# Performance work log

Hardware: AMD Instinct MI355X
Metric: run time of the kernel (lower is better)

## Reference

```python
import jax, jax.numpy as jnp
import numpy as np

B, T, V, N, H, L = 8, 512, 50257, 768, 12, 12
DH = N // H


def layernorm(x, w, eps=1e-5):
    mu = jnp.mean(x, axis=-1, keepdims=True)
    var = jnp.var(x, axis=-1, keepdims=True)
    return (x - mu) * jax.lax.rsqrt(var + eps) * w


def setup_inputs() -> dict:
    key = jax.random.key(0)
    ks = jax.random.split(key, 10)
    s = 0.02
    proj_s = 0.02 / np.sqrt(2.0)  # c_proj.weight special init (2 * n_layer, n_layer=1)
    return {
        "idx": jax.random.randint(ks[0], (B, T), 0, V),
        "wte": jax.random.normal(ks[1], (V, N), jnp.float32) * s,
        "wpe": jax.random.normal(ks[2], (T, N), jnp.float32) * s,
        "step_emb": jax.random.normal(ks[3], (L, N), jnp.float32) * s,
        "ln1_w": jnp.ones((N,), jnp.float32),
        "ln2_w": jnp.ones((N,), jnp.float32),
        "lnf_w": jnp.ones((N,), jnp.float32),
        "c_attn": jax.random.normal(ks[4], (N, 3 * N), jnp.float32) * s,
        "attn_proj": jax.random.normal(ks[5], (N, N), jnp.float32) * proj_s,
        "c_fc": jax.random.normal(ks[6], (N, 4 * N), jnp.float32) * s,
        "mlp_proj": jax.random.normal(ks[7], (4 * N, N), jnp.float32) * proj_s,
    }


def reference(idx, wte, wpe, step_emb, ln1_w, ln2_w, lnf_w, c_attn, attn_proj, c_fc, mlp_proj):
    b, t = idx.shape
    # token + position embeddings (dropout is identity in eval)
    x0 = wte[idx] + wpe[:t][None, :, :]  # [b, t, N]
    causal = jnp.tril(jnp.ones((t, t), dtype=bool))  # [t, t]
    neg_inf = jnp.finfo(x0.dtype).min

    def block(x):
        # causal self-attention
        h = layernorm(x, ln1_w)
        qkv = h @ c_attn  # [b, t, 3N]
        q, k, v = jnp.split(qkv, 3, axis=-1)
        q = q.reshape(b, t, H, DH)
        k = k.reshape(b, t, H, DH)
        v = v.reshape(b, t, H, DH)
        att = jnp.einsum('bqhd,bkhd->bhqk', q, k) / np.sqrt(DH)
        att = jnp.where(causal[None, None, :, :], att, neg_inf)
        att = jax.nn.softmax(att, axis=-1)
        y = jnp.einsum('bhqk,bkhd->bqhd', att, v).reshape(b, t, N)
        x = x + y @ attn_proj
        # MLP (exact GELU, matching torch nn.GELU default)
        m = layernorm(x, ln2_w)
        x = x + jax.nn.gelu(m @ c_fc, approximate=False) @ mlp_proj
        return x

    def step(h, se):
        h_in = h + x0 + se[None, None, :]
        return block(h_in), None

    h_final, _ = jax.lax.scan(step, x0, step_emb)  # loop num_loops times
    h_final = layernorm(h_final, lnf_w)
    # eval path with targets=None: logits only for last position, tied lm_head
    logits = h_final[:, -1:, :] @ wte.T  # [b, 1, V]
    return logits
```

## Files before the change

kernel.cpp:

```cpp
#include <hip/hip_runtime.h>
#include <hip/hip_bf16.h>
#include <math.h>

#define BB 8
#define TT 512
#define VV 50257
#define NN 768
#define HH 12
#define LL 12
#define MM (BB*TT)

typedef short bf16x8 __attribute__((ext_vector_type(8)));
typedef float f32x4 __attribute__((ext_vector_type(4)));
typedef unsigned short us8 __attribute__((ext_vector_type(8)));

__device__ __forceinline__ float bf2f(unsigned short u) {
    union { unsigned int i; float f; } x; x.i = ((unsigned int)u) << 16; return x.f;
}
__device__ __forceinline__ unsigned short f2bf(float f) {
    union { __hip_bfloat16 h; unsigned short u; } c; c.h = __float2bfloat16(f); return c.u;
}

__device__ __forceinline__ float gelu_f(float v) {
    float z = v * 0.70710678118654752f;
    float az = fabsf(z);
    float t = __builtin_amdgcn_rcpf(1.0f + 0.3275911f * az);
    float poly = t * (0.254829592f + t * (-0.284496736f + t * (1.421413741f
               + t * (-1.453152027f + t * 1.061405429f))));
    float erfa = 1.0f - poly * __expf(-z * z);
    float erfv = copysignf(erfa, z);
    return 0.5f * v * (1.0f + erfv);
}

__global__ __launch_bounds__(512) void embed_kernel(const int* __restrict__ idx,
                                                    const float* __restrict__ wte,
                                                    const float* __restrict__ wpe,
                                                    const float* __restrict__ se0,
                                                    float* __restrict__ x0,
                                                    float* __restrict__ hin)
{
    int row = blockIdx.x * 8 + (threadIdx.x >> 6);
    int lane = threadIdx.x & 63;
    int t = row % TT;
    int tok = idx[row];
    const float* wt = wte + (size_t)tok * NN;
    const float* wp = wpe + (size_t)t * NN;
    float* px = x0 + (size_t)row * NN;
    float* ph = hin + (size_t)row * NN;
#pragma unroll
    for (int i = 0; i < 3; ++i) {
        int c = (lane + i * 64) * 4;
        float4 a = *(const float4*)&wt[c];
        float4 b = *(const float4*)&wp[c];
        float4 e = *(const float4*)&se0[c];
        float4 v = make_float4(a.x + b.x, a.y + b.y, a.z + b.z, a.w + b.w);
        *(float4*)&px[c] = v;
        float4 h2 = make_float4(2.f * v.x + e.x, 2.f * v.y + e.y,
                                2.f * v.z + e.z, 2.f * v.w + e.w);
        *(float4*)&ph[c] = h2;
    }
}

__global__ __launch_bounds__(256) void wconv_all(
    const float* __restrict__ c_attn, const float* __restrict__ attn_proj,
    const float* __restrict__ c_fc, const float* __restrict__ mlp_proj,
    unsigned short* __restrict__ o1, unsigned short* __restrict__ o2,
    unsigned short* __restrict__ o3, unsigned short* __restrict__ o4)
{
    int bid = blockIdx.x;
    const float* W; unsigned short* Wt; int K, Nc, id;
    if (bid < 1728)      { W = c_attn;    Wt = o1; K = 768;  Nc = 2304; id = bid; }
    else if (bid < 2304) { W = attn_proj; Wt = o2; K = 768;  Nc = 768;  id = bid - 1728; }
    else if (bid < 4608) { W = c_fc;      Wt = o3; K = 768;  Nc = 3072; id = bid - 2304; }
    else                 { W = mlp_proj;  Wt = o4; K = 3072; Nc = 768;  id = bid - 4608; }
    int nbx = Nc / 32;
    int n0 = (id % nbx) * 32, k0 = (id / nbx) * 32;

    __shared__ float tile[32][33];
    int tid = threadIdx.x;
    int r = tid >> 3, c4 = (tid & 7) * 4;
    float4 v = *(const float4*)&W[(size_t)(k0 + r) * Nc + n0 + c4];
    tile[r][c4 + 0] = v.x; tile[r][c4 + 1] = v.y;
    tile[r][c4 + 2] = v.z; tile[r][c4 + 3] = v.w;
    __syncthreads();
    ushort4 o;
    o.x = f2bf(tile[c4 + 0][r]); o.y = f2bf(tile[c4 + 1][r]);
    o.z = f2bf(tile[c4 + 2][r]); o.w = f2bf(tile[c4 + 3][r]);
    *(ushort4*)&Wt[(size_t)(n0 + r) * K + k0 + c4] = o;
}

__global__ __launch_bounds__(512) void ln_kernel(
    const float* __restrict__ src, const float* __restrict__ w,
    unsigned short* __restrict__ out)
{
    int row = blockIdx.x * 8 + (threadIdx.x >> 6);
    int lane = threadIdx.x & 63;
    size_t base = (size_t)row * NN;
    float4 v[3];
    float s = 0.f, ss = 0.f;
#pragma unroll
    for (int i = 0; i < 3; ++i) {
        int c = (lane + i * 64) * 4;
        v[i] = *(const float4*)&src[base + c];
        s  += v[i].x + v[i].y + v[i].z + v[i].w;
        ss += v[i].x * v[i].x + v[i].y * v[i].y + v[i].z * v[i].z + v[i].w * v[i].w;
    }
#pragma unroll
    for (int off = 32; off; off >>= 1) { s += __shfl_xor(s, off); ss += __shfl_xor(ss, off); }
    float mu = s / (float)NN;
    float var = ss / (float)NN - mu * mu;
    float rsig = rsqrtf(var + 1e-5f);
#pragma unroll
    for (int i = 0; i < 3; ++i) {
        int c = (lane + i * 64) * 4;
        float4 wv = *(const float4*)&w[c];
        ushort4 u;
        u.x = f2bf((v[i].x - mu) * rsig * wv.x);
        u.y = f2bf((v[i].y - mu) * rsig * wv.y);
        u.z = f2bf((v[i].z - mu) * rsig * wv.z);
        u.w = f2bf((v[i].w - mu) * rsig * wv.w);
        *(ushort4*)&out[base + c] = u;
    }
}

template<int BN, int EPI, typename OutT>
__global__ __launch_bounds__(256) void mgemm(
    const unsigned short* __restrict__ A, const unsigned short* __restrict__ Bt,
    const float* __restrict__ res, OutT* __restrict__ C, int N, int K,
    const float* __restrict__ x0p, const float* __restrict__ sep)
{
    constexpr int NF = BN / 32;
    __shared__ unsigned short Asb[3][128 * 32];
    __shared__ unsigned short Bsb[3][BN * 32];
    int tid = threadIdx.x;

    int gx = gridDim.x, nwg = gx * gridDim.y;
    int bidl = blockIdx.y * gx + blockIdx.x;
    int cpx = nwg >> 3;
    int sbid = (bidl & 7) * cpx + (bidl >> 3);
    int bx = sbid % gx, by = sbid / gx;

    int row0 = by * 128, col0 = bx * BN;
    const unsigned short* Ap = A + (size_t)row0 * K;
    const unsigned short* Bp = Bt + (size_t)col0 * K;
    int lane = tid & 63, wid = tid >> 6;
    int wr = wid >> 1, wc = wid & 1;
    int fr = lane & 15, fq = lane >> 4;

    f32x4 acc[4][NF];
#pragma unroll
    for (int m = 0; m < 4; ++m)
#pragma unroll
        for (int n = 0; n < NF; ++n)
#pragma unroll
            for (int r = 0; r < 4; ++r) acc[m][n][r] = 0.f;

    int ldso = (tid & 192) * 8;

    auto STAGE = [&](int buf, int k0) {
#pragma unroll
        for (int i = 0; i < 2; ++i) {
            int c = i * 256 + tid;
            __builtin_amdgcn_global_load_lds(
                (const __attribute__((address_space(1))) void*)(Ap + (size_t)(c >> 2) * K + k0 + (c & 3) * 8),
                (__attribute__((address_space(3))) void*)(Asb[buf] + i * 2048 + ldso), 16, 0, 0);
        }
        if constexpr (BN == 128) {
#pragma unroll
            for (int i = 0; i < 2; ++i) {
                int c = i * 256 + tid;
                __builtin_amdgcn_global_load_lds(
                    (const __attribute__((address_space(1))) void*)(Bp + (size_t)(c >> 2) * K + k0 + (c & 3) * 8),
                    (__attribute__((address_space(3))) void*)(Bsb[buf] + i * 2048 + ldso), 16, 0, 0);
            }
        } else {
            __builtin_amdgcn_global_load_lds(
                (const __attribute__((address_space(1))) void*)(Bp + (size_t)(tid >> 2) * K + k0 + (tid & 3) * 8),
                (__attribute__((address_space(3))) void*)(Bsb[buf] + ldso), 16, 0, 0);
        }
    };

    auto COMPUTE = [&](int buf) {
        const unsigned short* Ab = Asb[buf] + (wr * 64 + fr) * 32 + fq * 8;
        const unsigned short* Bb = Bsb[buf] + (wc * (BN / 2) + fr) * 32 + fq * 8;
        bf16x8 af[4], bfr[NF];
#pragma unroll
        for (int m = 0; m < 4; ++m) af[m] = *(const bf16x8*)(Ab + m * 512);
#pragma unroll
        for (int n = 0; n < NF; ++n) bfr[n] = *(const bf16x8*)(Bb + n * 512);
        __builtin_amdgcn_s_setprio(1);
#pragma unroll
        for (int m = 0; m < 4; ++m)
#pragma unroll
            for (int n = 0; n < NF; ++n)
                acc[m][n] = __builtin_amdgcn_mfma_f32_16x16x32_bf16(af[m], bfr[n], acc[m][n], 0, 0, 0);
        __builtin_amdgcn_s_setprio(0);
    };

    int NT = K / 32;
    STAGE(0, 0);
    for (int t = 0; t < NT; ++t) {
        if (t + 1 < NT) {
            STAGE((t + 1) % 3, (t + 1) * 32);
            if constexpr (BN == 128) asm volatile("s_waitcnt vmcnt(4)" ::: "memory");
            else                     asm volatile("s_waitcnt vmcnt(3)" ::: "memory");
        } else {
            asm volatile("s_waitcnt vmcnt(0)" ::: "memory");
        }
        __builtin_amdgcn_s_barrier();
        COMPUTE(t % 3);
    }

#pragma unroll
    for (int m = 0; m < 4; ++m) {
#pragma unroll
        for (int n = 0; n < NF; ++n) {
            int col = col0 + wc * (BN / 2) + n * 16 + fr;
#pragma unroll
            for (int r = 0; r < 4; ++r) {
                int row = row0 + wr * 64 + m * 16 + fq * 4 + r;
                float v = acc[m][n][r];
                if (EPI == 1) v = gelu_f(v);
                if (EPI == 2) v += res[(size_t)row * N + col];
                if (EPI == 3) v += res[(size_t)row * N + col] + x0p[(size_t)row * N + col] + sep[col];
                if constexpr (sizeof(OutT) == 2) C[(size_t)row * N + col] = (OutT)f2bf(v);
                else C[(size_t)row * N + col] = v;
            }
        }
    }
}

__global__ __launch_bounds__(512) void fattn_kernel(const unsigned short* __restrict__ qkv,
                                                    unsigned short* __restrict__ y)
{
    int qt = blockIdx.x, h = blockIdx.y, b = blockIdx.z;
    int tid = threadIdx.x, lane = tid & 63, w = tid >> 6;
    int fr = lane & 15, fq = lane >> 4;

    __shared__ unsigned short Ks[2][64 * 72];
    __shared__ unsigned short Vts[2][64 * 72];
    __shared__ unsigned short Ps[128 * 72];

    int qrow = qt * 128 + w * 16 + fr;
    const unsigned short* qp = qkv + (size_t)(b * TT + qrow) * 2304 + h * 64 + fq * 8;
    bf16x8 qf0 = *(const bf16x8*)qp;
    bf16x8 qf1 = *(const bf16x8*)(qp + 32);

    bool kside = tid < 256;
    int st = tid & 255;
    int sr = st >> 2, sc = (st & 3) * 16;
    const unsigned short* gsrc = qkv + (size_t)(b * TT + sr) * 2304 + (kside ? 768 : 1536) + h * 64 + sc;

    f32x4 acco[4];
#pragma unroll
    for (int n = 0; n < 4; ++n)
#pragma unroll
        for (int r = 0; r < 4; ++r) acco[n][r] = 0.f;
    float lrow = 0.f;

    us8 r0, r1;
    {
        const us8* p = (const us8*)gsrc;
        r0 = p[0]; r1 = p[1];
        if (kside) {
            *(us8*)&Ks[0][sr * 72 + sc] = r0;
            *(us8*)&Ks[0][sr * 72 + sc + 8] = r1;
        } else {
#pragma unroll
            for (int i = 0; i < 8; ++i) {
                int d0 = sc + i, d1 = sc + 8 + i;
                Vts[0][d0 * 72 + (sr ^ (((d0 >> 4) & 3) << 4))] = r0[i];
                Vts[0][d1 * 72 + (sr ^ (((d1 >> 4) & 3) << 4))] = r1[i];
            }
        }
    }
    __syncthreads();

    int qmax = qt * 128 + w * 16 + 15;
    int NTk = 2 * qt + 2;
    for (int kt = 0; kt < NTk; ++kt) {
        int cur = kt & 1;
        bool pre = (kt + 1 < NTk);
        if (pre) {
            const us8* p = (const us8*)(gsrc + (size_t)(kt + 1) * 64 * 2304);
            r0 = p[0]; r1 = p[1];
        }

        if (kt * 64 <= qmax) {
            f32x4 accs[4];
#pragma unroll
            for (int n = 0; n < 4; ++n)
#pragma unroll
                for (int r = 0; r < 4; ++r) accs[n][r] = 0.f;
            {
                bf16x8 kf0[4], kf1[4];
#pragma unroll
                for (int n = 0; n < 4; ++n) {
                    kf0[n] = *(const bf16x8*)&Ks[cur][(n * 16 + fr) * 72 + fq * 8];
                    kf1[n] = *(const bf16x8*)&Ks[cur][(n * 16 + fr) * 72 + 32 + fq * 8];
                }
                __builtin_amdgcn_s_setprio(1);
#pragma unroll
                for (int n = 0; n < 4; ++n) {
                    accs[n] = __builtin_amdgcn_mfma_f32_16x16x32_bf16(kf0[n], qf0, accs[n], 0, 0, 0);
                    accs[n] = __builtin_amdgcn_mfma_f32_16x16x32_bf16(kf1[n], qf1, accs[n], 0, 0, 0);
                }
                __builtin_amdgcn_s_setprio(0);
            }

            bool diag = (kt * 64 + 63 > qt * 128 + w * 16);
#pragma unroll
            for (int n = 0; n < 4; ++n) {
                ushort4 pw;
                unsigned short* pwp = (unsigned short*)&pw;
#pragma unroll
                for (int r = 0; r < 4; ++r) {
                    float s = accs[n][r] * 0.125f;
                    if (diag) { int j = kt * 64 + n * 16 + fq * 4 + r; if (j > qrow) s = -1e30f; }
                    float p = __expf(s);
                    lrow += p;
                    pwp[r] = f2bf(p);
                }
                *(ushort4*)&Ps[(w * 16 + fr) * 72 + n * 16 + fq * 4] = pw;
            }

            {
                bf16x8 pf0 = *(const bf16x8*)&Ps[(w * 16 + fr) * 72 + fq * 8];
                bf16x8 pf1 = *(const bf16x8*)&Ps[(w * 16 + fr) * 72 + 32 + fq * 8];
                bf16x8 vf0[4], vf1[4];
#pragma unroll
                for (int n = 0; n < 4; ++n) {
                    int cA = (fq * 8) ^ (n << 4);
                    int cB = (32 + fq * 8) ^ (n << 4);
                    vf0[n] = *(const bf16x8*)&Vts[cur][(n * 16 + fr) * 72 + cA];
                    vf1[n] = *(const bf16x8*)&Vts[cur][(n * 16 + fr) * 72 + cB];
                }
                __builtin_amdgcn_s_setprio(1);
#pragma unroll
                for (int n = 0; n < 4; ++n) {
                    acco[n] = __builtin_amdgcn_mfma_f32_16x16x32_bf16(vf0[n], pf0, acco[n], 0, 0, 0);
                    acco[n] = __builtin_amdgcn_mfma_f32_16x16x32_bf16(vf1[n], pf1, acco[n], 0, 0, 0);
                }
                __builtin_amdgcn_s_setprio(0);
            }
        }

        if (pre) {
            if (kside) {
                *(us8*)&Ks[cur ^ 1][sr * 72 + sc] = r0;
                *(us8*)&Ks[cur ^ 1][sr * 72 + sc + 8] = r1;
            } else {
#pragma unroll
                for (int i = 0; i < 8; ++i) {
                    int d0 = sc + i, d1 = sc + 8 + i;
                    Vts[cur ^ 1][d0 * 72 + (sr ^ (((d0 >> 4) & 3) << 4))] = r0[i];
                    Vts[cur ^ 1][d1 * 72 + (sr ^ (((d1 >> 4) & 3) << 4))] = r1[i];
                }
            }
        }
        __syncthreads();
    }

    lrow += __shfl_xor(lrow, 16);
    lrow += __shfl_xor(lrow, 32);
    float inv = 1.0f / lrow;

    unsigned short* yp = y + (size_t)(b * TT + qrow) * NN + h * 64;
#pragma unroll
    for (int n = 0; n < 4; ++n) {
        ushort4 u;
        u.x = f2bf(acco[n][0] * inv);
        u.y = f2bf(acco[n][1] * inv);
        u.z = f2bf(acco[n][2] * inv);
        u.w = f2bf(acco[n][3] * inv);
        *(ushort4*)&yp[n * 16 + fq * 4] = u;
    }
}

__global__ __launch_bounds__(256) void logits_kernel(const float* __restrict__ hf,
                                                     const float* __restrict__ lnw,
                                                     const float* __restrict__ wte,
                                                     float* __restrict__ out)
{
    __shared__ float hl[BB][NN];
    int wv = threadIdx.x >> 6, lane = threadIdx.x & 63;
    for (int rr = wv; rr < BB; rr += 4) {
        const float* src = hf + (size_t)(rr * TT + TT - 1) * NN;
        float4 v[3]; float s = 0.f, ss = 0.f;
#pragma unroll
        for (int i = 0; i < 3; ++i) {
            int c = (lane + i * 64) * 4;
            v[i] = *(const float4*)&src[c];
            s  += v[i].x + v[i].y + v[i].z + v[i].w;
            ss += v[i].x * v[i].x + v[i].y * v[i].y + v[i].z * v[i].z + v[i].w * v[i].w;
        }
#pragma unroll
        for (int off = 32; off; off >>= 1) { s += __shfl_xor(s, off); ss += __shfl_xor(ss, off); }
        float mu = s / (float)NN;
        float rsig = rsqrtf(ss / (float)NN - mu * mu + 1e-5f);
#pragma unroll
        for (int i = 0; i < 3; ++i) {
            int c = (lane + i * 64) * 4;
            float4 wv4 = *(const float4*)&lnw[c];
            float4 o;
            o.x = (v[i].x - mu) * rsig * wv4.x;
            o.y = (v[i].y - mu) * rsig * wv4.y;
            o.z = (v[i].z - mu) * rsig * wv4.z;
            o.w = (v[i].w - mu) * rsig * wv4.w;
            *(float4*)&hl[rr][c] = o;
        }
    }
    __syncthreads();

    const int NCH = (VV + 3) / 4;
    for (int cid = blockIdx.x * 4 + wv; cid < NCH; cid += gridDim.x * 4) {
        int v0 = cid * 4;
        float4 wv4[4][3];
#pragma unroll
        for (int r = 0; r < 4; ++r) {
            int v = min(v0 + r, VV - 1);
            const float4* wr4 = (const float4*)(wte + (size_t)v * NN);
#pragma unroll
            for (int i = 0; i < 3; ++i) wv4[r][i] = wr4[i * 64 + lane];
        }
        float acc[4][BB];
#pragma unroll
        for (int r = 0; r < 4; ++r)
#pragma unroll
            for (int b = 0; b < BB; ++b) acc[r][b] = 0.f;
#pragma unroll
        for (int i = 0; i < 3; ++i) {
#pragma unroll
            for (int b = 0; b < BB; ++b) {
                float4 h4 = *(const float4*)&hl[b][i * 256 + lane * 4];
#pragma unroll
                for (int r = 0; r < 4; ++r)
                    acc[r][b] += wv4[r][i].x * h4.x + wv4[r][i].y * h4.y
                               + wv4[r][i].z * h4.z + wv4[r][i].w * h4.w;
            }
        }
#pragma unroll
        for (int off = 32; off; off >>= 1)
#pragma unroll
            for (int r = 0; r < 4; ++r)
#pragma unroll
                for (int b = 0; b < BB; ++b) acc[r][b] += __shfl_xor(acc[r][b], off);
        if (lane == 0) {
#pragma unroll
            for (int r = 0; r < 4; ++r) {
                int v = v0 + r;
                if (v < VV)
#pragma unroll
                    for (int b = 0; b < BB; ++b) out[(size_t)b * VV + v] = acc[r][b];
            }
        }
    }
}

extern "C" void kernel_launch(void* const* d_in, const int* in_sizes, int n_in,
                              void* d_out, int out_size, void* d_ws, size_t ws_size,
                              hipStream_t stream) {
    const int*   idx       = (const int*)d_in[0];
    const float* wte       = (const float*)d_in[1];
    const float* wpe       = (const float*)d_in[2];
    const float* step_emb  = (const float*)d_in[3];
    const float* ln1_w     = (const float*)d_in[4];
    const float* ln2_w     = (const float*)d_in[5];
    const float* lnf_w     = (const float*)d_in[6];
    const float* c_attn    = (const float*)d_in[7];
    const float* attn_proj = (const float*)d_in[8];
    const float* c_fc      = (const float*)d_in[9];
    const float* mlp_proj  = (const float*)d_in[10];
    float* out = (float*)d_out;

    float* ws = (float*)d_ws;
    const size_t RC = (size_t)MM * NN;
    float* x0  = ws;
    float* hin = ws + RC;
    unsigned short* big = (unsigned short*)(ws + 2 * RC);
    unsigned short* lnb = (unsigned short*)(ws + 2 * RC + (size_t)MM * 3072 / 2);
    unsigned short* yb       = lnb + RC;
    unsigned short* cattn_bt = yb + RC;
    unsigned short* aproj_bt = cattn_bt + (size_t)2304 * 768;
    unsigned short* cfc_bt   = aproj_bt + (size_t)768 * 768;
    unsigned short* mproj_bt = cfc_bt + (size_t)768 * 3072;

    wconv_all<<<6912, 256, 0, stream>>>(c_attn, attn_proj, c_fc, mlp_proj,
                                        cattn_bt, aproj_bt, cfc_bt, mproj_bt);

    embed_kernel<<<MM / 8, 512, 0, stream>>>(idx, wte, wpe, step_emb, x0, hin);

    for (int l = 0; l < LL; ++l) {
        ln_kernel<<<MM / 8, 512, 0, stream>>>(hin, ln1_w, lnb);
        mgemm<128, 0, unsigned short><<<dim3(2304 / 128, MM / 128), 256, 0, stream>>>(
            lnb, cattn_bt, nullptr, big, 2304, 768, nullptr, nullptr);
        fattn_kernel<<<dim3(TT / 128, HH, BB), 512, 0, stream>>>(big, yb);
        mgemm<64, 2, float><<<dim3(768 / 64, MM / 128), 256, 0, stream>>>(
            yb, aproj_bt, hin, hin, 768, 768, nullptr, nullptr);
        ln_kernel<<<MM / 8, 512, 0, stream>>>(hin, ln2_w, lnb);
        mgemm<128, 1, unsigned short><<<dim3(3072 / 128, MM / 128), 256, 0, stream>>>(
            lnb, cfc_bt, nullptr, big, 3072, 768, nullptr, nullptr);
        if (l + 1 < LL) {
            mgemm<64, 3, float><<<dim3(768 / 64, MM / 128), 256, 0, stream>>>(
                big, mproj_bt, hin, hin, 768, 3072, x0, step_emb + (l + 1) * NN);
        } else {
            mgemm<64, 2, float><<<dim3(768 / 64, MM / 128), 256, 0, stream>>>(
                big, mproj_bt, hin, hin, 768, 3072, nullptr, nullptr);
        }
    }

    logits_kernel<<<1024, 256, 0, stream>>>(hin, lnf_w, wte, out);
}
```

Before: 1.821 ms.

## Fold layernorm into GEMMs via weight-scaled columns and epilogue row statistics

Removes the two standalone layernorm kernels per layer. The LN weight is folded into the bf16 transposed weights, and per-column sums of the weights are precomputed. The preceding GEMM epilogues (and the embedding kernel) emit a bf16 copy of the residual plus partial row sum and sum-of-squares. The next GEMM then applies the mean and rstd correction in its epilogue as acc*rsig - rsig*mu*colsum. This saves a full read/write pass over activations twice per layer, at the cost of extra epilogue stores, an extra LDS reduction, and precision loss because the raw un-normalized residual is quantized to bf16 before the matmul.

```diff
diff --git a/kernel.cpp b/kernel.cpp
--- a/kernel.cpp
+++ b/kernel.cpp
@@ -37,7 +37,9 @@
                                                     const float* __restrict__ wpe,
                                                     const float* __restrict__ se0,
                                                     float* __restrict__ x0,
-                                                    float* __restrict__ hin)
+                                                    float* __restrict__ hin,
+                                                    unsigned short* __restrict__ hinb,
+                                                    float* __restrict__ pln1)
 {
     int row = blockIdx.x * 8 + (threadIdx.x >> 6);
     int lane = threadIdx.x & 63;
@@ -47,6 +49,8 @@
     const float* wp = wpe + (size_t)t * NN;
     float* px = x0 + (size_t)row * NN;
     float* ph = hin + (size_t)row * NN;
+    unsigned short* phb = hinb + (size_t)row * NN;
+    float s = 0.f, ss = 0.f;
 #pragma unroll
     for (int i = 0; i < 3; ++i) {
         int c = (lane + i * 64) * 4;
@@ -58,21 +62,33 @@
         float4 h2 = make_float4(2.f * v.x + e.x, 2.f * v.y + e.y,
                                 2.f * v.z + e.z, 2.f * v.w + e.w);
         *(float4*)&ph[c] = h2;
+        ushort4 u;
+        u.x = f2bf(h2.x); u.y = f2bf(h2.y); u.z = f2bf(h2.z); u.w = f2bf(h2.w);
+        *(ushort4*)&phb[c] = u;
+        s  += h2.x + h2.y + h2.z + h2.w;
+        ss += h2.x * h2.x + h2.y * h2.y + h2.z * h2.z + h2.w * h2.w;
+    }
+#pragma unroll
+    for (int off = 32; off; off >>= 1) { s += __shfl_xor(s, off); ss += __shfl_xor(ss, off); }
+    if (lane < 12) {
+        float2 pv = (lane == 0) ? make_float2(s, ss) : make_float2(0.f, 0.f);
+        *(float2*)&pln1[(size_t)row * 24 + lane * 2] = pv;
     }
 }
 
 __global__ __launch_bounds__(256) void wconv_all(
     const float* __restrict__ c_attn, const float* __restrict__ attn_proj,
     const float* __restrict__ c_fc, const float* __restrict__ mlp_proj,
+    const float* __restrict__ ln1w, const float* __restrict__ ln2w,
     unsigned short* __restrict__ o1, unsigned short* __restrict__ o2,
     unsigned short* __restrict__ o3, unsigned short* __restrict__ o4)
 {
     int bid = blockIdx.x;
-    const float* W; unsigned short* Wt; int K, Nc, id;
-    if (bid < 1728)      { W = c_attn;    Wt = o1; K = 768;  Nc = 2304; id = bid; }
-    else if (bid < 2304) { W = attn_proj; Wt = o2; K = 768;  Nc = 768;  id = bid - 1728; }
-    else if (bid < 4608) { W = c_fc;      Wt = o3; K = 768;  Nc = 3072; id = bid - 2304; }
-    else                 { W = mlp_proj;  Wt = o4; K = 3072; Nc = 768;  id = bid - 4608; }
+    const float* W; unsigned short* Wt; const float* wf; int K, Nc, id;
+    if (bid < 1728)      { W = c_attn;    Wt = o1; wf = ln1w;    K = 768;  Nc = 2304; id = bid; }
+    else if (bid < 2304) { W = attn_proj; Wt = o2; wf = nullptr; K = 768;  Nc = 768;  id = bid - 1728; }
+    else if (bid < 4608) { W = c_fc;      Wt = o3; wf = ln2w;    K = 768;  Nc = 3072; id = bid - 2304; }
+    else                 { W = mlp_proj;  Wt = o4; wf = nullptr; K = 3072; Nc = 768;  id = bid - 4608; }
     int nbx = Nc / 32;
     int n0 = (id % nbx) * 32, k0 = (id / nbx) * 32;
 
@@ -83,55 +99,49 @@
     tile[r][c4 + 0] = v.x; tile[r][c4 + 1] = v.y;
     tile[r][c4 + 2] = v.z; tile[r][c4 + 3] = v.w;
     __syncthreads();
+    float w0 = 1.f, w1 = 1.f, w2 = 1.f, w3 = 1.f;
+    if (wf) { w0 = wf[k0 + c4]; w1 = wf[k0 + c4 + 1]; w2 = wf[k0 + c4 + 2]; w3 = wf[k0 + c4 + 3]; }
     ushort4 o;
-    o.x = f2bf(tile[c4 + 0][r]); o.y = f2bf(tile[c4 + 1][r]);
-    o.z = f2bf(tile[c4 + 2][r]); o.w = f2bf(tile[c4 + 3][r]);
+    o.x = f2bf(tile[c4 + 0][r] * w0); o.y = f2bf(tile[c4 + 1][r] * w1);
+    o.z = f2bf(tile[c4 + 2][r] * w2); o.w = f2bf(tile[c4 + 3][r] * w3);
     *(ushort4*)&Wt[(size_t)(n0 + r) * K + k0 + c4] = o;
 }
 
-__global__ __launch_bounds__(512) void ln_kernel(
-    const float* __restrict__ src, const float* __restrict__ w,
-    unsigned short* __restrict__ out)
+__global__ __launch_bounds__(256) void colsum_kernel(const float* __restrict__ c_attn,
+                                                     const float* __restrict__ c_fc,
+                                                     const float* __restrict__ w1,
+                                                     const float* __restrict__ w2,
+                                                     float* __restrict__ Sa,
+                                                     float* __restrict__ Sf)
 {
-    int row = blockIdx.x * 8 + (threadIdx.x >> 6);
-    int lane = threadIdx.x & 63;
-    size_t base = (size_t)row * NN;
-    float4 v[3];
-    float s = 0.f, ss = 0.f;
-#pragma unroll
-    for (int i = 0; i < 3; ++i) {
-        int c = (lane + i * 64) * 4;
-        v[i] = *(const float4*)&src[base + c];
-        s  += v[i].x + v[i].y + v[i].z + v[i].w;
-        ss += v[i].x * v[i].x + v[i].y * v[i].y + v[i].z * v[i].z + v[i].w * v[i].w;
-    }
-#pragma unroll
-    for (int off = 32; off; off >>= 1) { s += __shfl_xor(s, off); ss += __shfl_xor(ss, off); }
-    float mu = s / (float)NN;
-    float var = ss / (float)NN - mu * mu;
-    float rsig = rsqrtf(var + 1e-5f);
-#pragma unroll
-    for (int i = 0; i < 3; ++i) {
-        int c = (lane + i * 64) * 4;
-        float4 wv = *(const float4*)&w[c];
-        ushort4 u;
-        u.x = f2bf((v[i].x - mu) * rsig * wv.x);
-        u.y = f2bf((v[i].y - mu) * rsig * wv.y);
-        u.z = f2bf((v[i].z - mu) * rsig * wv.z);
-        u.w = f2bf((v[i].w - mu) * rsig * wv.w);
-        *(ushort4*)&out[base + c] = u;
-    }
-}
-
-template<int BN, int EPI, typename OutT>
+    int n = blockIdx.x * 256 + threadIdx.x;
+    if (n < 2304) {
+        float s = 0.f;
+        for (int k = 0; k < 768; ++k) s += w1[k] * c_attn[(size_t)k * 2304 + n];
+        Sa[n] = s;
+    } else {
+        int nn = n - 2304;
+        float s = 0.f;
+        for (int k = 0; k < 768; ++k) s += w2[k] * c_fc[(size_t)k * 3072 + nn];
+        Sf[nn] = s;
+    }
+}
+
+template<int BN, int EPI, int WST, typename OutT>
 __global__ __launch_bounds__(256) void mgemm(
     const unsigned short* __restrict__ A, const unsigned short* __restrict__ Bt,
     const float* __restrict__ res, OutT* __restrict__ C, int N, int K,
-    const float* __restrict__ x0p, const float* __restrict__ sep)
+    const float* __restrict__ x0p, const float* __restrict__ sep,
+    const float* __restrict__ plnIn, const float* __restrict__ Svec,
+    float* __restrict__ pout, unsigned short* __restrict__ hb)
 {
     constexpr int NF = BN / 32;
-    __shared__ unsigned short Asb[3][128 * 32];
-    __shared__ unsigned short Bsb[3][BN * 32];
+    constexpr int ASZ = 3 * 128 * 32;
+    constexpr int BSZ = 3 * BN * 32;
+    __shared__ unsigned short SMEM[ASZ + BSZ];
+    __shared__ float2 fstats[128];
+    unsigned short* AsbF = SMEM;
+    unsigned short* BsbF = SMEM + ASZ;
     int tid = threadIdx.x;
 
     int gx = gridDim.x, nwg = gx * gridDim.y;
@@ -147,6 +157,19 @@
     int wr = wid >> 1, wc = wid & 1;
     int fr = lane & 15, fq = lane >> 4;
 
+    if constexpr (EPI >= 4) {
+        if (tid < 128) {
+            const float2* pp = (const float2*)(plnIn + (size_t)(row0 + tid) * 24);
+            float S = 0.f, SS = 0.f;
+#pragma unroll
+            for (int j = 0; j < 12; ++j) { float2 e = pp[j]; S += e.x; SS += e.y; }
+            float mu = S * (1.0f / 768.0f);
+            float var = SS * (1.0f / 768.0f) - mu * mu;
+            float rsig = rsqrtf(var + 1e-5f);
+            fstats[tid] = make_float2(rsig, rsig * mu);
+        }
+    }
+
     f32x4 acc[4][NF];
 #pragma unroll
     for (int m = 0; m < 4; ++m)
@@ -163,7 +186,7 @@
             int c = i * 256 + tid;
             __builtin_amdgcn_global_load_lds(
                 (const __attribute__((address_space(1))) void*)(Ap + (size_t)(c >> 2) * K + k0 + (c & 3) * 8),
-                (__attribute__((address_space(3))) void*)(Asb[buf] + i * 2048 + ldso), 16, 0, 0);
+                (__attribute__((address_space(3))) void*)(AsbF + buf * 4096 + i * 2048 + ldso), 16, 0, 0);
         }
         if constexpr (BN == 128) {
 #pragma unroll
@@ -171,18 +194,18 @@
                 int c = i * 256 + tid;
                 __builtin_amdgcn_global_load_lds(
                     (const __attribute__((address_space(1))) void*)(Bp + (size_t)(c >> 2) * K + k0 + (c & 3) * 8),
-                    (__attribute__((address_space(3))) void*)(Bsb[buf] + i * 2048 + ldso), 16, 0, 0);
+                    (__attribute__((address_space(3))) void*)(BsbF + buf * (BN * 32) + i * 2048 + ldso), 16, 0, 0);
             }
         } else {
             __builtin_amdgcn_global_load_lds(
                 (const __attribute__((address_space(1))) void*)(Bp + (size_t)(tid >> 2) * K + k0 + (tid & 3) * 8),
-                (__attribute__((address_space(3))) void*)(Bsb[buf] + ldso), 16, 0, 0);
+                (__attribute__((address_space(3))) void*)(BsbF + buf * (BN * 32) + ldso), 16, 0, 0);
         }
     };
 
     auto COMPUTE = [&](int buf) {
-        const unsigned short* Ab = Asb[buf] + (wr * 64 + fr) * 32 + fq * 8;
-        const unsigned short* Bb = Bsb[buf] + (wc * (BN / 2) + fr) * 32 + fq * 8;
+        const unsigned short* Ab = AsbF + buf * 4096 + (wr * 64 + fr) * 32 + fq * 8;
+        const unsigned short* Bb = BsbF + buf * (BN * 32) + (wc * (BN / 2) + fr) * 32 + fq * 8;
         bf16x8 af[4], bfr[NF];
 #pragma unroll
         for (int m = 0; m < 4; ++m) af[m] = *(const bf16x8*)(Ab + m * 512);
@@ -211,20 +234,74 @@
         COMPUTE(t % 3);
     }
 
-#pragma unroll
-    for (int m = 0; m < 4; ++m) {
-#pragma unroll
-        for (int n = 0; n < NF; ++n) {
-            int col = col0 + wc * (BN / 2) + n * 16 + fr;
-#pragma unroll
-            for (int r = 0; r < 4; ++r) {
-                int row = row0 + wr * 64 + m * 16 + fq * 4 + r;
-                float v = acc[m][n][r];
-                if (EPI == 1) v = gelu_f(v);
-                if (EPI == 2) v += res[(size_t)row * N + col];
-                if (EPI == 3) v += res[(size_t)row * N + col] + x0p[(size_t)row * N + col] + sep[col];
-                if constexpr (sizeof(OutT) == 2) C[(size_t)row * N + col] = (OutT)f2bf(v);
-                else C[(size_t)row * N + col] = v;
+    if constexpr (EPI >= 4) {
+        float2 stv[4][4];
+#pragma unroll
+        for (int m = 0; m < 4; ++m)
+#pragma unroll
+            for (int r = 0; r < 4; ++r)
+                stv[m][r] = fstats[wr * 64 + m * 16 + fq * 4 + r];
+#pragma unroll
+        for (int m = 0; m < 4; ++m) {
+#pragma unroll
+            for (int n = 0; n < NF; ++n) {
+                int col = col0 + wc * (BN / 2) + n * 16 + fr;
+                float sv = Svec[col];
+#pragma unroll
+                for (int r = 0; r < 4; ++r) {
+                    int row = row0 + wr * 64 + m * 16 + fq * 4 + r;
+                    float v = acc[m][n][r] * stv[m][r].x - stv[m][r].y * sv;
+                    if (EPI == 5) v = gelu_f(v);
+                    C[(size_t)row * N + col] = (OutT)f2bf(v);
+                }
+            }
+        }
+    } else {
+        float p[4][4], q[4][4];
+        if constexpr (WST) {
+#pragma unroll
+            for (int m = 0; m < 4; ++m)
+#pragma unroll
+                for (int r = 0; r < 4; ++r) { p[m][r] = 0.f; q[m][r] = 0.f; }
+        }
+#pragma unroll
+        for (int m = 0; m < 4; ++m) {
+#pragma unroll
+            for (int n = 0; n < NF; ++n) {
+                int col = col0 + wc * (BN / 2) + n * 16 + fr;
+#pragma unroll
+                for (int r = 0; r < 4; ++r) {
+                    int row = row0 + wr * 64 + m * 16 + fq * 4 + r;
+                    float v = acc[m][n][r];
+                    if (EPI == 1) v = gelu_f(v);
+                    if (EPI == 2) v += res[(size_t)row * N + col];
+                    if (EPI == 3) v += res[(size_t)row * N + col] + x0p[(size_t)row * N + col] + sep[col];
+                    if constexpr (sizeof(OutT) == 2) C[(size_t)row * N + col] = (OutT)f2bf(v);
+                    else C[(size_t)row * N + col] = v;
+                    if constexpr (WST) {
+                        hb[(size_t)row * N + col] = f2bf(v);
+                        p[m][r] += v;
+                        q[m][r] += v * v;
+                    }
+                }
+            }
+        }
+        if constexpr (WST) {
+            __syncthreads();
+            float2* red = (float2*)SMEM;
+#pragma unroll
+            for (int m = 0; m < 4; ++m)
+#pragma unroll
+                for (int r = 0; r < 4; ++r) {
+                    int lr = wr * 64 + m * 16 + fq * 4 + r;
+                    red[lr * 33 + fr * 2 + wc] = make_float2(p[m][r], q[m][r]);
+                }
+            __syncthreads();
+            if (tid < 128) {
+                float S = 0.f, SS = 0.f;
+#pragma unroll
+                for (int j = 0; j < 32; ++j) { float2 e = red[tid * 33 + j]; S += e.x; SS += e.y; }
+                *(float2*)&pout[(size_t)(row0 + tid) * 24 + bx * 2] = make_float2(S, SS);
             }
         }
     }
@@ -475,37 +552,39 @@
 
     float* ws = (float*)d_ws;
     const size_t RC = (size_t)MM * NN;
-    float* x0  = ws;
-    float* hin = ws + RC;
-    unsigned short* big = (unsigned short*)(ws + 2 * RC);
-    unsigned short* lnb = (unsigned short*)(ws + 2 * RC + (size_t)MM * 3072 / 2);
-    unsigned short* yb       = lnb + RC;
-    unsigned short* cattn_bt = yb + RC;
+    float* x0   = ws;
+    float* hin  = ws + RC;
+    float* Sa   = ws + 2 * RC;
+    float* Sf   = Sa + 2304;
+    float* pln1 = Sf + 3072;
+    float* pln2 = pln1 + (size_t)MM * 24;
+    unsigned short* big  = (unsigned short*)(pln2 + (size_t)MM * 24);
+    unsigned short* yb   = big + (size_t)MM * 3072;
+    unsigned short* hinb = yb + RC;
+    unsigned short* cattn_bt = hinb + RC;
     unsigned short* aproj_bt = cattn_bt + (size_t)2304 * 768;
     unsigned short* cfc_bt   = aproj_bt + (size_t)768 * 768;
     unsigned short* mproj_bt = cfc_bt + (size_t)768 * 3072;
 
-    wconv_all<<<6912, 256, 0, stream>>>(c_attn, attn_proj, c_fc, mlp_proj,
+    wconv_all<<<6912, 256, 0, stream>>>(c_attn, attn_proj, c_fc, mlp_proj, ln1_w, ln2_w,
                                         cattn_bt, aproj_bt, cfc_bt, mproj_bt);
-
-    embed_kernel<<<MM / 8, 512, 0, stream>>>(idx, wte, wpe, step_emb, x0, hin);
+    colsum_kernel<<<21, 256, 0, stream>>>(c_attn, c_fc, ln1_w, ln2_w, Sa, Sf);
+    embed_kernel<<<MM / 8, 512, 0, stream>>>(idx, wte, wpe, step_emb, x0, hin, hinb, pln1);
 
     for (int l = 0; l < LL; ++l) {
-        ln_kernel<<<MM / 8, 512, 0, stream>>>(hin, ln1_w, lnb);
-        mgemm<128, 0, unsigned short><<<dim3(2304 / 128, MM / 128), 256, 0, stream>>>(
-            lnb, cattn_bt, nullptr, big, 2304, 768, nullptr, nullptr);
+        mgemm<128, 4, 0, unsigned short><<<dim3(2304 / 128, MM / 128), 256, 0, stream>>>(
+            hinb, cattn_bt, nullptr, big, 2304, 768, nullptr, nullptr, pln1, Sa, nullptr, nullptr);
         fattn_kernel<<<dim3(TT / 128, HH, BB), 512, 0, stream>>>(big, yb);
-        mgemm<64, 2, float><<<dim3(768 / 64, MM / 128), 256, 0, stream>>>(
-            yb, aproj_bt, hin, hin, 768, 768, nullptr, nullptr);
-        ln_kernel<<<MM / 8, 512, 0, stream>>>(hin, ln2_w, lnb);
-        mgemm<128, 1, unsigned short><<<dim3(3072 / 128, MM / 128), 256, 0, stream>>>(
-            lnb, cfc_bt, nullptr, big, 3072, 768, nullptr, nullptr);
+        mgemm<64, 2, 1, float><<<dim3(768 / 64, MM / 128), 256, 0, stream>>>(
+            yb, aproj_bt, hin, hin, 768, 768, nullptr, nullptr, nullptr, nullptr, pln2, hinb);
+        mgemm<128, 5, 0, unsigned short><<<dim3(3072 / 128, MM / 128), 256, 0, stream>>>(
+            hinb, cfc_bt, nullptr, big, 3072, 768, nullptr, nullptr, pln2, Sf, nullptr, nullptr);
         if (l + 1 < LL) {
-            mgemm<64, 3, float><<<dim3(768 / 64, MM / 128), 256, 0, stream>>>(
-                big, mproj_bt, hin, hin, 768, 3072, x0, step_emb + (l + 1) * NN);
+            mgemm<64, 3, 1, float><<<dim3(768 / 64, MM / 128), 256, 0, stream>>>(
+                big, mproj_bt, hin, hin, 768, 3072, x0, step_emb + (l + 1) * NN, nullptr, nullptr, pln1, hinb);
         } else {
-            mgemm<64, 2, float><<<dim3(768 / 64, MM / 128), 256, 0, stream>>>(
-                big, mproj_bt, hin, hin, 768, 3072, nullptr, nullptr);
+            mgemm<64, 2, 0, float><<<dim3(768 / 64, MM / 128), 256, 0, stream>>>(
+                big, mproj_bt, hin, hin, 768, 3072, nullptr, nullptr, nullptr, nullptr, nullptr, nullptr);
         }
     }
 
```

Measured after the change: 1.929 ms. 1.06x slower.
